# Performance work log

Hardware: AMD Instinct MI355X
Metric: run time of the kernel (lower is better)

Reference implementation:

```python
import jax, jax.numpy as jnp
import numpy as np

# Fixed-step Dormand-Prince (DOPRI5) 5th-order solution over t in [0, 1].
# The original uses tfp's adaptive DormandPrince with first_step_size=0.01 and
# rtol=atol=1e-4; a data-dependent adaptive loop is not a usable correctness
# baseline, so we integrate with the same tableau at a fixed dt=0.01 (100 steps),
# which matches the adaptive solution to well within the solver tolerance for
# these smooth tanh-MLP dynamics.

DT = 0.01
N_STEPS = 100
BATCH, D_MODEL, HIDDEN = 32768, 128, 128


def setup_inputs() -> dict:
    key = jax.random.key(0)
    k1, k2, k3 = jax.random.split(key, 3)
    x = jax.random.normal(k1, (BATCH, D_MODEL), dtype=jnp.float32)
    W1 = jax.random.normal(k2, (D_MODEL, HIDDEN), dtype=jnp.float32) / np.sqrt(D_MODEL)
    b1 = jnp.zeros((HIDDEN,), dtype=jnp.float32)
    W2 = jax.random.normal(k3, (HIDDEN, D_MODEL), dtype=jnp.float32) * (0.05 / np.sqrt(HIDDEN))
    b2 = jnp.zeros((D_MODEL,), dtype=jnp.float32)
    return {"x": x, "W1": W1, "b1": b1, "W2": W2, "b2": b2}


def reference(x, W1, b1, W2, b2):
    def f(y):  # autonomous odefunc: tanh MLP
        return jnp.tanh(y @ W1 + b1) @ W2 + b2

    def dopri_step(y, _):
        k1 = f(y)
        k2 = f(y + DT * (1.0 / 5.0) * k1)
        k3 = f(y + DT * (3.0 / 40.0 * k1 + 9.0 / 40.0 * k2))
        k4 = f(y + DT * (44.0 / 45.0 * k1 - 56.0 / 15.0 * k2 + 32.0 / 9.0 * k3))
        k5 = f(y + DT * (19372.0 / 6561.0 * k1 - 25360.0 / 2187.0 * k2
                         + 64448.0 / 6561.0 * k3 - 212.0 / 729.0 * k4))
        k6 = f(y + DT * (9017.0 / 3168.0 * k1 - 355.0 / 33.0 * k2
                         + 46732.0 / 5247.0 * k3 + 49.0 / 176.0 * k4
                         - 5103.0 / 18656.0 * k5))
        y_new = y + DT * (35.0 / 384.0 * k1 + 500.0 / 1113.0 * k3
                          + 125.0 / 192.0 * k4 - 2187.0 / 6784.0 * k5
                          + 11.0 / 84.0 * k6)
        return y_new, None

    y_final, _ = jax.lax.scan(dopri_step, x, None, length=N_STEPS)
    return y_final.astype(jnp.float32)
```

## Files before the change

### kernel.cpp

```cpp
#include <hip/hip_runtime.h>


#define DT 0.01f
#define N_STEPS 100
#define LDS_STRIDE 136

typedef __attribute__((ext_vector_type(8))) short short8;
typedef __attribute__((ext_vector_type(4))) float f32x4;

__device__ __forceinline__ unsigned short f2bf(float f) {
  unsigned u = __builtin_bit_cast(unsigned, f);
  u += 0x7fffu + ((u >> 16) & 1u);
  return (unsigned short)(u >> 16);
}

__device__ __forceinline__ float fast_tanh(float x) {
  float xc = fminf(fmaxf(x, -9.f), 9.f);
  float e = __expf(2.f * xc);
  return 1.f - 2.f * __builtin_amdgcn_rcpf(e + 1.f);
}

template <typename ZF, typename KF>
__device__ __forceinline__ void feval(unsigned short* zb, const unsigned short* w1t,
                                      const short8 (&w2f)[8][4], const float (&bias1)[8],
                                      const float (&bias2)[8], int kg, int ln, ZF zfun,
                                      KF kfun) {
#pragma unroll
  for (int nt = 0; nt < 8; nt++)
#pragma unroll
    for (int r = 0; r < 4; r++)
      zb[(4 * kg + r) * LDS_STRIDE + nt * 16 + ln] = f2bf(zfun(nt * 4 + r));

  short8 af[4];
#pragma unroll
  for (int ks = 0; ks < 4; ks++)
    af[ks] = *(const short8*)&zb[ln * LDS_STRIDE + ks * 32 + kg * 8];

#pragma unroll
  for (int nt = 0; nt < 8; nt++) {
    f32x4 acc = {0.f, 0.f, 0.f, 0.f};
#pragma unroll
    for (int ks = 0; ks < 4; ks++) {
      short8 bfrag = *(const short8*)&w1t[(nt * 16 + ln) * LDS_STRIDE + ks * 32 + kg * 8];
      acc = __builtin_amdgcn_mfma_f32_16x16x32_bf16(af[ks], bfrag, acc, 0, 0, 0);
    }
#pragma unroll
    for (int r = 0; r < 4; r++)
      zb[(4 * kg + r) * LDS_STRIDE + nt * 16 + ln] = f2bf(fast_tanh(acc[r] + bias1[nt]));
  }

#pragma unroll
  for (int ks = 0; ks < 4; ks++)
    af[ks] = *(const short8*)&zb[ln * LDS_STRIDE + ks * 32 + kg * 8];

#pragma unroll
  for (int nt = 0; nt < 8; nt++) {
    f32x4 acc = {0.f, 0.f, 0.f, 0.f};
#pragma unroll
    for (int ks = 0; ks < 4; ks++)
      acc = __builtin_amdgcn_mfma_f32_16x16x32_bf16(af[ks], w2f[nt][ks], acc, 0, 0, 0);
#pragma unroll
    for (int r = 0; r < 4; r++) kfun(nt * 4 + r, acc[r] + bias2[nt]);
  }
}

__global__ __launch_bounds__(256, 1) void ode_kernel(const float* __restrict__ x,
                                                     const float* __restrict__ W1,
                                                     const float* __restrict__ b1,
                                                     const float* __restrict__ W2,
                                                     const float* __restrict__ b2,
                                                     float* __restrict__ out) {
  __shared__ unsigned short w1t[128 * LDS_STRIDE];
  __shared__ unsigned short zb_all[4][16 * LDS_STRIDE];

  const int tid = threadIdx.x;
  const int wave = tid >> 6;
  const int lane = tid & 63;
  const int ln = lane & 15;
  const int kg = lane >> 4;

  for (int i = tid; i < 128 * 128; i += 256) {
    int k = i >> 7, n = i & 127;
    w1t[n * LDS_STRIDE + k] = f2bf(W1[i]);
  }
  __syncthreads();

  short8 w2f[8][4];
#pragma unroll
  for (int nt = 0; nt < 8; nt++)
#pragma unroll
    for (int ks = 0; ks < 4; ks++) {
      short8 v;
#pragma unroll
      for (int j = 0; j < 8; j++)
        v[j] = (short)f2bf(W2[(ks * 32 + kg * 8 + j) * 128 + nt * 16 + ln]);
      w2f[nt][ks] = v;
    }

  float bias1[8], bias2[8];
#pragma unroll
  for (int nt = 0; nt < 8; nt++) {
    bias1[nt] = b1[nt * 16 + ln];
    bias2[nt] = b2[nt * 16 + ln];
  }

  unsigned short* zb = &zb_all[wave][0];
  const int rowbase = blockIdx.x * 64 + wave * 16;

  float y[32], k1[32], k2[32], k3[32], k4[32], k5[32];
#pragma unroll
  for (int nt = 0; nt < 8; nt++)
#pragma unroll
    for (int r = 0; r < 4; r++)
      y[nt * 4 + r] = x[(rowbase + 4 * kg + r) * 128 + nt * 16 + ln];

#pragma unroll 1
  for (int step = 0; step < N_STEPS; step++) {
    feval(zb, w1t, w2f, bias1, bias2, kg, ln,
          [&](int i) { return y[i]; },
          [&](int i, float kv) { k1[i] = kv; });
    feval(zb, w1t, w2f, bias1, bias2, kg, ln,
          [&](int i) { return y[i] + DT * (0.2f * k1[i]); },
          [&](int i, float kv) { k2[i] = kv; });
    feval(zb, w1t, w2f, bias1, bias2, kg, ln,
          [&](int i) {
            return y[i] + DT * ((3.f / 40.f) * k1[i] + (9.f / 40.f) * k2[i]);
          },
          [&](int i, float kv) { k3[i] = kv; });
    feval(zb, w1t, w2f, bias1, bias2, kg, ln,
          [&](int i) {
            return y[i] + DT * ((44.f / 45.f) * k1[i] - (56.f / 15.f) * k2[i] +
                                (32.f / 9.f) * k3[i]);
          },
          [&](int i, float kv) { k4[i] = kv; });
    feval(zb, w1t, w2f, bias1, bias2, kg, ln,
          [&](int i) {
            return y[i] + DT * ((19372.f / 6561.f) * k1[i] - (25360.f / 2187.f) * k2[i] +
                                (64448.f / 6561.f) * k3[i] - (212.f / 729.f) * k4[i]);
          },
          [&](int i, float kv) { k5[i] = kv; });
    feval(zb, w1t, w2f, bias1, bias2, kg, ln,
          [&](int i) {
            return y[i] + DT * ((9017.f / 3168.f) * k1[i] - (355.f / 33.f) * k2[i] +
                                (46732.f / 5247.f) * k3[i] + (49.f / 176.f) * k4[i] -
                                (5103.f / 18656.f) * k5[i]);
          },
          [&](int i, float kv) {
            y[i] += DT * ((35.f / 384.f) * k1[i] + (500.f / 1113.f) * k3[i] +
                          (125.f / 192.f) * k4[i] - (2187.f / 6784.f) * k5[i] +
                          (11.f / 84.f) * kv);
          });
  }

#pragma unroll
  for (int nt = 0; nt < 8; nt++)
#pragma unroll
    for (int r = 0; r < 4; r++)
      out[(rowbase + 4 * kg + r) * 128 + nt * 16 + ln] = y[nt * 4 + r];
}

extern "C" void kernel_launch(void* const* d_in, const int* in_sizes, int n_in,
                              void* d_out, int out_size, void* d_ws, size_t ws_size,
                              hipStream_t stream) {
  const float* x = (const float*)d_in[0];
  const float* W1 = (const float*)d_in[1];
  const float* b1 = (const float*)d_in[2];
  const float* W2 = (const float*)d_in[3];
  const float* b2 = (const float*)d_in[4];
  float* out = (float*)d_out;

  dim3 grid(512), block(256);
  hipLaunchKernelGGL(ode_kernel, grid, block, 0, stream, x, W1, b1, W2, b2, out);
}
```

Before: 3.426 ms.

## Move W2 fragments from registers to LDS and double waves per block

W2 is now kept transposed in bf16 in shared memory and read per MFMA, instead of being held as 128 VGPRs per lane. This lowers register pressure so the kernel can use 512-thread blocks with a launch bound of 2 blocks per CU, giving more waves to hide MFMA and tanh latency. The grid is halved to 256 blocks of 128 rows each. In exchange every feval issues extra LDS reads for W2, and shared memory use roughly doubles per block, which may limit how many blocks fit on a CU.

```diff
diff --git a/kernel.cpp b/kernel.cpp
--- a/kernel.cpp
+++ b/kernel.cpp
@@ -3,7 +3,7 @@
 
 #define DT 0.01f
 #define N_STEPS 100
-#define LDS_STRIDE 136
+#define W1S 136
 
 typedef __attribute__((ext_vector_type(8))) short short8;
 typedef __attribute__((ext_vector_type(4))) float f32x4;
@@ -21,57 +21,62 @@
 }
 
 template <typename ZF, typename KF>
-__device__ __forceinline__ void feval(unsigned short* zb, const unsigned short* w1t,
-                                      const short8 (&w2f)[8][4], const float (&bias1)[8],
-                                      const float (&bias2)[8], int kg, int ln, ZF zfun,
-                                      KF kfun) {
+__device__ __forceinline__ void feval(unsigned short* zb,
+                                      const unsigned short* w1t,
+                                      const unsigned short* w2t,
+                                      const float (&bias1)[8],
+                                      const float (&bias2)[8], int kg, int ln,
+                                      ZF zfun, KF kfun) {
 #pragma unroll
   for (int nt = 0; nt < 8; nt++)
 #pragma unroll
     for (int r = 0; r < 4; r++)
-      zb[(4 * kg + r) * LDS_STRIDE + nt * 16 + ln] = f2bf(zfun(nt * 4 + r));
+      zb[(4 * kg + r) * W1S + nt * 16 + ln] = f2bf(zfun(nt * 4 + r));
 
   short8 af[4];
 #pragma unroll
   for (int ks = 0; ks < 4; ks++)
-    af[ks] = *(const short8*)&zb[ln * LDS_STRIDE + ks * 32 + kg * 8];
+    af[ks] = *(const short8*)&zb[ln * W1S + ks * 32 + kg * 8];
 
 #pragma unroll
   for (int nt = 0; nt < 8; nt++) {
     f32x4 acc = {0.f, 0.f, 0.f, 0.f};
 #pragma unroll
     for (int ks = 0; ks < 4; ks++) {
-      short8 bfrag = *(const short8*)&w1t[(nt * 16 + ln) * LDS_STRIDE + ks * 32 + kg * 8];
+      short8 bfrag = *(const short8*)&w1t[(nt * 16 + ln) * W1S + ks * 32 + kg * 8];
       acc = __builtin_amdgcn_mfma_f32_16x16x32_bf16(af[ks], bfrag, acc, 0, 0, 0);
     }
 #pragma unroll
     for (int r = 0; r < 4; r++)
-      zb[(4 * kg + r) * LDS_STRIDE + nt * 16 + ln] = f2bf(fast_tanh(acc[r] + bias1[nt]));
+      zb[(4 * kg + r) * W1S + nt * 16 + ln] =
+          f2bf(fast_tanh(acc[r] + bias1[nt]));
   }
 
+  short8 ah[4];
 #pragma unroll
   for (int ks = 0; ks < 4; ks++)
-    af[ks] = *(const short8*)&zb[ln * LDS_STRIDE + ks * 32 + kg * 8];
+    ah[ks] = *(const short8*)&zb[ln * W1S + ks * 32 + kg * 8];
 
 #pragma unroll
   for (int nt = 0; nt < 8; nt++) {
     f32x4 acc = {0.f, 0.f, 0.f, 0.f};
 #pragma unroll
-    for (int ks = 0; ks < 4; ks++)
-      acc = __builtin_amdgcn_mfma_f32_16x16x32_bf16(af[ks], w2f[nt][ks], acc, 0, 0, 0);
+    for (int ks = 0; ks < 4; ks++) {
+      short8 bfrag = *(const short8*)&w2t[(nt * 16 + ln) * W1S + ks * 32 + kg * 8];
+      acc = __builtin_amdgcn_mfma_f32_16x16x32_bf16(ah[ks], bfrag, acc, 0, 0, 0);
+    }
 #pragma unroll
     for (int r = 0; r < 4; r++) kfun(nt * 4 + r, acc[r] + bias2[nt]);
   }
 }
 
-__global__ __launch_bounds__(256, 1) void ode_kernel(const float* __restrict__ x,
-                                                     const float* __restrict__ W1,
-                                                     const float* __restrict__ b1,
-                                                     const float* __restrict__ W2,
-                                                     const float* __restrict__ b2,
-                                                     float* __restrict__ out) {
-  __shared__ unsigned short w1t[128 * LDS_STRIDE];
-  __shared__ unsigned short zb_all[4][16 * LDS_STRIDE];
+__global__ __launch_bounds__(512, 2) void ode_kernel(
+    const float* __restrict__ x, const float* __restrict__ W1,
+    const float* __restrict__ b1, const float* __restrict__ W2,
+    const float* __restrict__ b2, float* __restrict__ out) {
+  __shared__ unsigned short w1t[128 * W1S];
+  __shared__ unsigned short w2t[128 * W1S];
+  __shared__ unsigned short zb_all[8][16 * W1S];
 
   const int tid = threadIdx.x;
   const int wave = tid >> 6;
@@ -79,23 +84,12 @@
   const int ln = lane & 15;
   const int kg = lane >> 4;
 
-  for (int i = tid; i < 128 * 128; i += 256) {
+  for (int i = tid; i < 128 * 128; i += 512) {
     int k = i >> 7, n = i & 127;
-    w1t[n * LDS_STRIDE + k] = f2bf(W1[i]);
+    w1t[n * W1S + k] = f2bf(W1[i]);
+    w2t[n * W1S + k] = f2bf(W2[i]);
   }
   __syncthreads();
-
-  short8 w2f[8][4];
-#pragma unroll
-  for (int nt = 0; nt < 8; nt++)
-#pragma unroll
-    for (int ks = 0; ks < 4; ks++) {
-      short8 v;
-#pragma unroll
-      for (int j = 0; j < 8; j++)
-        v[j] = (short)f2bf(W2[(ks * 32 + kg * 8 + j) * 128 + nt * 16 + ln]);
-      w2f[nt][ks] = v;
-    }
 
   float bias1[8], bias2[8];
 #pragma unroll
@@ -105,7 +99,7 @@
   }
 
   unsigned short* zb = &zb_all[wave][0];
-  const int rowbase = blockIdx.x * 64 + wave * 16;
+  const int rowbase = blockIdx.x * 128 + wave * 16;
 
   float y[32], k1[32], k2[32], k3[32], k4[32], k5[32];
 #pragma unroll
@@ -116,33 +110,37 @@
 
 #pragma unroll 1
   for (int step = 0; step < N_STEPS; step++) {
-    feval(zb, w1t, w2f, bias1, bias2, kg, ln,
+    feval(zb, w1t, w2t, bias1, bias2, kg, ln,
           [&](int i) { return y[i]; },
           [&](int i, float kv) { k1[i] = kv; });
-    feval(zb, w1t, w2f, bias1, bias2, kg, ln,
+    feval(zb, w1t, w2t, bias1, bias2, kg, ln,
           [&](int i) { return y[i] + DT * (0.2f * k1[i]); },
           [&](int i, float kv) { k2[i] = kv; });
-    feval(zb, w1t, w2f, bias1, bias2, kg, ln,
+    feval(zb, w1t, w2t, bias1, bias2, kg, ln,
           [&](int i) {
             return y[i] + DT * ((3.f / 40.f) * k1[i] + (9.f / 40.f) * k2[i]);
           },
           [&](int i, float kv) { k3[i] = kv; });
-    feval(zb, w1t, w2f, bias1, bias2, kg, ln,
+    feval(zb, w1t, w2t, bias1, bias2, kg, ln,
           [&](int i) {
             return y[i] + DT * ((44.f / 45.f) * k1[i] - (56.f / 15.f) * k2[i] +
                                 (32.f / 9.f) * k3[i]);
           },
           [&](int i, float kv) { k4[i] = kv; });
-    feval(zb, w1t, w2f, bias1, bias2, kg, ln,
+    feval(zb, w1t, w2t, bias1, bias2, kg, ln,
           [&](int i) {
-            return y[i] + DT * ((19372.f / 6561.f) * k1[i] - (25360.f / 2187.f) * k2[i] +
-                                (64448.f / 6561.f) * k3[i] - (212.f / 729.f) * k4[i]);
+            return y[i] + DT * ((19372.f / 6561.f) * k1[i] -
+                                (25360.f / 2187.f) * k2[i] +
+                                (64448.f / 6561.f) * k3[i] -
+                                (212.f / 729.f) * k4[i]);
           },
           [&](int i, float kv) { k5[i] = kv; });
-    feval(zb, w1t, w2f, bias1, bias2, kg, ln,
+    feval(zb, w1t, w2t, bias1, bias2, kg, ln,
           [&](int i) {
-            return y[i] + DT * ((9017.f / 3168.f) * k1[i] - (355.f / 33.f) * k2[i] +
-                                (46732.f / 5247.f) * k3[i] + (49.f / 176.f) * k4[i] -
+            return y[i] + DT * ((9017.f / 3168.f) * k1[i] -
+                                (355.f / 33.f) * k2[i] +
+                                (46732.f / 5247.f) * k3[i] +
+                                (49.f / 176.f) * k4[i] -
                                 (5103.f / 18656.f) * k5[i]);
           },
           [&](int i, float kv) {
@@ -160,8 +158,8 @@
 }
 
 extern "C" void kernel_launch(void* const* d_in, const int* in_sizes, int n_in,
-                              void* d_out, int out_size, void* d_ws, size_t ws_size,
-                              hipStream_t stream) {
+                              void* d_out, int out_size, void* d_ws,
+                              size_t ws_size, hipStream_t stream) {
   const float* x = (const float*)d_in[0];
   const float* W1 = (const float*)d_in[1];
   const float* b1 = (const float*)d_in[2];
@@ -169,6 +167,7 @@
   const float* b2 = (const float*)d_in[4];
   float* out = (float*)d_out;
 
-  dim3 grid(512), block(256);
-  hipLaunchKernelGGL(ode_kernel, grid, block, 0, stream, x, W1, b1, W2, b2, out);
+  dim3 grid(256), block(512);
+  hipLaunchKernelGGL(ode_kernel, grid, block, 0, stream, x, W1, b1, W2, b2,
+                     out);
 }
```

New measurement: 11.60 ms. 239% more time.
